# Optimization experiments

Measured on AMD Instinct MI355X. Metric: run time of the kernel, lower is better.

The kernel has to match this reference:

```python
import jax, jax.numpy as jnp
import numpy as np

H, KVH, HD, HID = 16, 8, 128, 2048
GROUPS = H // KVH
THETA = 10000.0
EPS = 1e-6


def _rms_norm(x, w):
    # x: (..., HD), norm in fp32 like Qwen3RMSNorm
    xf = x.astype(jnp.float32)
    var = jnp.mean(xf * xf, axis=-1, keepdims=True)
    return (xf * jax.lax.rsqrt(var + EPS)).astype(x.dtype) * w


def _rope_cos_sin(position_ids, dtype):
    # position_ids: (B, S) int
    inv_freq = 1.0 / (THETA ** (jnp.arange(0, HD, 2, dtype=jnp.float32) / HD))  # (HD/2,)
    freqs = position_ids.astype(jnp.float32)[..., None] * inv_freq  # (B, S, HD/2)
    emb = jnp.concatenate([freqs, freqs], axis=-1)  # (B, S, HD)
    return jnp.cos(emb).astype(dtype), jnp.sin(emb).astype(dtype)


def _rotate_half(x):
    x1, x2 = jnp.split(x, 2, axis=-1)
    return jnp.concatenate([-x2, x1], axis=-1)


def _apply_rope(q, k, cos, sin):
    # q,k: (B, h, S, HD); cos,sin: (B, S, HD) -> broadcast over head dim
    cos = cos[:, None, :, :]
    sin = sin[:, None, :, :]
    q = q * cos + _rotate_half(q) * sin
    k = k * cos + _rotate_half(k) * sin
    return q, k


def setup_inputs() -> dict:
    key = jax.random.key(0)
    ks = jax.random.split(key, 10)
    B, S, L = 1, 2048, 2048
    w = 0.02
    return {
        "hidden_states": jax.random.normal(ks[0], (B, S, HID), jnp.float32),
        "context": jax.random.normal(ks[1], (B, L, HID), jnp.float32),
        "position_ids": jnp.arange(S, dtype=jnp.int64)[None, :].repeat(B, axis=0),
        "Wq": jax.random.normal(ks[2], (H * HD, HID), jnp.float32) * w,
        "Wk": jax.random.normal(ks[3], (KVH * HD, HID), jnp.float32) * w,
        "Wv": jax.random.normal(ks[4], (KVH * HD, HID), jnp.float32) * w,
        "Wo": jax.random.normal(ks[5], (HID, H * HD), jnp.float32) * w,
        "Wk_ctx": jax.random.normal(ks[6], (KVH * HD, HID), jnp.float32) * w,
        "Wv_ctx": jax.random.normal(ks[7], (KVH * HD, HID), jnp.float32) * w,
        "q_norm_w": jnp.ones((HD,), jnp.float32),
        "k_norm_w": jnp.ones((HD,), jnp.float32),
    }


def reference(hidden_states, context, position_ids, Wq, Wk, Wv, Wo, Wk_ctx, Wv_ctx, q_norm_w, k_norm_w):
    B, S, _ = hidden_states.shape
    L = context.shape[1]
    scaling = HD ** -0.5

    Q = (hidden_states @ Wq.T).reshape(B, S, H, HD).transpose(0, 2, 1, 3)    # (B,H,S,HD)
    K = (hidden_states @ Wk.T).reshape(B, S, KVH, HD).transpose(0, 2, 1, 3)  # (B,KVH,S,HD)
    V = (hidden_states @ Wv.T).reshape(B, S, KVH, HD).transpose(0, 2, 1, 3)

    Q = _rms_norm(Q, q_norm_w)
    K = _rms_norm(K, k_norm_w)

    cos, sin = _rope_cos_sin(position_ids, Q.dtype)
    Q, K = _apply_rope(Q, K, cos, sin)

    K_ctx = (context @ Wk_ctx.T).reshape(B, L, KVH, HD).transpose(0, 2, 1, 3)
    V_ctx = (context @ Wv_ctx.T).reshape(B, L, KVH, HD).transpose(0, 2, 1, 3)

    K_full = jnp.concatenate([K_ctx, K], axis=2)  # (B,KVH,L+S,HD)
    V_full = jnp.concatenate([V_ctx, V], axis=2)
    K_full = jnp.repeat(K_full, GROUPS, axis=1)   # (B,H,L+S,HD)
    V_full = jnp.repeat(V_full, GROUPS, axis=1)

    attn = jnp.einsum("bhsd,bhtd->bhst", Q, K_full) * scaling  # (B,H,S,L+S)
    attn = jax.nn.softmax(attn.astype(jnp.float32), axis=-1).astype(Q.dtype)
    out = jnp.einsum("bhst,bhtd->bhsd", attn, V_full)          # (B,H,S,HD)
    out = out.transpose(0, 2, 1, 3).reshape(B, S, H * HD)
    return out @ Wo.T
```

## Files before the change

### kernel.cpp

```cpp
#include <hip/hip_runtime.h>

typedef __bf16 bf16_t;
typedef __attribute__((ext_vector_type(8))) __bf16 bf16x8;
typedef __attribute__((ext_vector_type(4))) __bf16 bf16x4;
typedef __attribute__((ext_vector_type(4))) float f32x4;

#define LDA_PAD 72

__device__ __forceinline__ bf16x8 ld8(const float* g) {
  f32x4 a = *(const f32x4*)g;
  f32x4 b = *(const f32x4*)(g + 4);
  bf16x8 r;
  r[0] = (bf16_t)a[0]; r[1] = (bf16_t)a[1]; r[2] = (bf16_t)a[2]; r[3] = (bf16_t)a[3];
  r[4] = (bf16_t)b[0]; r[5] = (bf16_t)b[1]; r[6] = (bf16_t)b[2]; r[7] = (bf16_t)b[3];
  return r;
}
__device__ __forceinline__ bf16x8 ld8(const bf16_t* g) { return *(const bf16x8*)g; }

__global__ __launch_bounds__(256) void cvt_wo(const float* __restrict__ src,
                                              bf16_t* __restrict__ dst) {
  const size_t off = (size_t)(blockIdx.x * 256 + threadIdx.x) * 8;
  *(bf16x8*)(dst + off) = ld8(src + off);
}

template<typename TI>
__global__ __launch_bounds__(256) void proj_all(
    const TI* __restrict__ hs, const TI* __restrict__ ctx,
    const TI* __restrict__ Wq, const TI* __restrict__ Wk,
    const TI* __restrict__ Wv, const TI* __restrict__ Wkc,
    const TI* __restrict__ Wvc,
    bf16_t* __restrict__ Qb, bf16_t* __restrict__ Kb, bf16_t* __restrict__ Vt)
{
  __shared__ __align__(16) bf16_t lA[128 * LDA_PAD];
  __shared__ __align__(16) bf16_t lB[128 * LDA_PAD];
  const int tid = threadIdx.x, wave = tid >> 6, lane = tid & 63;
  const int quad = lane >> 4, lc = lane & 15;
  const int u = blockIdx.x;
  const int xcd = u & 7, v = u >> 3;
  const int op = v >> 5, w = v & 31;
  const int nh = w >> 4, mt0 = w & 15;
  const int n0 = (xcd + nh * 8) * 128, m0 = mt0 * 128;
  const TI* A; const TI* B;
  if (op == 0) { A = hs; B = Wq + (size_t)n0 * 2048; }
  else {
    A = (op == 1) ? ctx : hs;
    const TI* WK = (op == 1) ? Wkc : Wk;
    const TI* WV = (op == 1) ? Wvc : Wv;
    B = (n0 < 1024) ? WK + (size_t)n0 * 2048 : WV + (size_t)(n0 - 1024) * 2048;
  }
  const int mw = (wave >> 1) * 64, nw = (wave & 1) * 64;
  const int lr8 = lane >> 3, lc8 = (lane & 7) * 8;

  f32x4 acc[4][4];
#pragma unroll
  for (int i = 0; i < 4; ++i)
#pragma unroll
    for (int j = 0; j < 4; ++j) acc[i][j] = (f32x4){0.f, 0.f, 0.f, 0.f};

  bf16x8 pa[4], pb[4];
#pragma unroll
  for (int i = 0; i < 4; ++i) {
    const int row = (wave + 4 * i) * 8 + lr8;
    pa[i] = ld8(A + (size_t)(m0 + row) * 2048 + lc8);
    pb[i] = ld8(B + (size_t)row * 2048 + lc8);
  }

  for (int k0 = 0; k0 < 2048; k0 += 64) {
    __syncthreads();
#pragma unroll
    for (int i = 0; i < 4; ++i) {
      const int row = (wave + 4 * i) * 8 + lr8;
      *(bf16x8*)(lA + row * LDA_PAD + lc8) = pa[i];
      *(bf16x8*)(lB + row * LDA_PAD + lc8) = pb[i];
    }
    __syncthreads();
    if (k0 + 64 < 2048) {
      const int kn = k0 + 64;
#pragma unroll
      for (int i = 0; i < 4; ++i) {
        const int row = (wave + 4 * i) * 8 + lr8;
        pa[i] = ld8(A + (size_t)(m0 + row) * 2048 + kn + lc8);
        pb[i] = ld8(B + (size_t)row * 2048 + kn + lc8);
      }
    }
#pragma unroll
    for (int kk = 0; kk < 2; ++kk) {
      bf16x8 af[4], bfv[4];
#pragma unroll
      for (int mt = 0; mt < 4; ++mt)
        af[mt] = *(const bf16x8*)(lA + (mw + mt * 16 + lc) * LDA_PAD + kk * 32 + quad * 8);
#pragma unroll
      for (int nt = 0; nt < 4; ++nt)
        bfv[nt] = *(const bf16x8*)(lB + (nw + nt * 16 + lc) * LDA_PAD + kk * 32 + quad * 8);
#pragma unroll
      for (int mt = 0; mt < 4; ++mt)
#pragma unroll
        for (int nt = 0; nt < 4; ++nt)
          acc[mt][nt] = __builtin_amdgcn_mfma_f32_16x16x32_bf16(af[mt], bfv[nt], acc[mt][nt], 0, 0, 0);
    }
  }

  if (op == 0) {
#pragma unroll
    for (int mt = 0; mt < 4; ++mt)
#pragma unroll
      for (int nt = 0; nt < 4; ++nt)
#pragma unroll
        for (int r = 0; r < 4; ++r)
          Qb[(size_t)(m0 + mw + mt * 16 + quad * 4 + r) * 2048 + n0 + nw + nt * 16 + lc]
              = (bf16_t)acc[mt][nt][r];
  } else {
    const int t_off = (op == 1) ? 0 : 2048;
    if (n0 < 1024) {
#pragma unroll
      for (int mt = 0; mt < 4; ++mt)
#pragma unroll
        for (int nt = 0; nt < 4; ++nt)
#pragma unroll
          for (int r = 0; r < 4; ++r) {
            const int n = n0 + nw + nt * 16 + lc;
            const int kvh = n >> 7, dd = n & 127;
            const int t = t_off + m0 + mw + mt * 16 + quad * 4 + r;
            Kb[((size_t)kvh * 4096 + t) * 128 + dd] = (bf16_t)acc[mt][nt][r];
          }
    } else {
#pragma unroll
      for (int mt = 0; mt < 4; ++mt)
#pragma unroll
        for (int nt = 0; nt < 4; ++nt) {
          const int n = n0 - 1024 + nw + nt * 16 + lc;
          const int kvh = n >> 7, dd = n & 127;
          const int t = t_off + m0 + mw + mt * 16 + quad * 4;
          bf16x4 pk;
#pragma unroll
          for (int r = 0; r < 4; ++r) pk[r] = (bf16_t)acc[mt][nt][r];
          *(bf16x4*)(Vt + ((size_t)kvh * 128 + dd) * 4096 + t) = pk;
        }
    }
  }
}

__global__ __launch_bounds__(256) void normrope(
    bf16_t* __restrict__ Q, bf16_t* __restrict__ Kb,
    const float* __restrict__ qw, const float* __restrict__ kw)
{
  const int wave = threadIdx.x >> 6, lane = threadIdx.x & 63;
  const int row = blockIdx.x * 4 + wave;
  bf16_t* p; const float* w; int pos;
  if (row < 32768) {
    const int s = row >> 4, hh = row & 15;
    p = Q + (size_t)s * 2048 + hh * 128; w = qw; pos = s;
  } else {
    const int rk = row - 32768;
    const int s = rk >> 3, hh = rk & 7;
    p = Kb + ((size_t)hh * 4096 + 2048 + s) * 128; w = kw; pos = s;
  }
  const float x1 = (float)p[lane], x2 = (float)p[lane + 64];
  float ss = x1 * x1 + x2 * x2;
#pragma unroll
  for (int m = 1; m < 64; m <<= 1) ss += __shfl_xor(ss, m, 64);
  const float inv = rsqrtf(ss * (1.0f / 128.0f) + 1e-6f);
  const float y1 = x1 * inv * w[lane];
  const float y2 = x2 * inv * w[lane + 64];
  const float freq = (float)pos * exp2f((float)lane * (-13.287712379549449f / 64.0f));
  const float cb = cosf(freq), sb = sinf(freq);
  p[lane]      = (bf16_t)(y1 * cb - y2 * sb);
  p[lane + 64] = (bf16_t)(y2 * cb + y1 * sb);
}

template<int SPLIT>
__global__ __launch_bounds__(512, 4) void attn_kernel(
    const bf16_t* __restrict__ Q, const bf16_t* __restrict__ Kb,
    const bf16_t* __restrict__ Vt, bf16_t* __restrict__ O,
    float* __restrict__ Of, float* __restrict__ Lf)
{
  __shared__ __align__(16) char lK[64 * 256];
  __shared__ __align__(16) char lV[128 * 128];
  __shared__ __align__(16) char lP[8 * 2048];
  const int tid = threadIdx.x, wave = tid >> 6, lane = tid & 63;
  const int quad = lane >> 4, lc = lane & 15;
  const int bid = blockIdx.x;
  const int hk = bid & 7, qt = (bid >> 3) & 15, hsel = (bid >> 7) & 1;
  const int half = SPLIT ? (bid >> 8) : 0;
  const int h = hk * 2 + hsel;
  const int mrow0 = qt * 128 + wave * 16;
  const int tbase = half * 2048;
  const int tend = tbase + (SPLIT ? 2048 : 4096);
  const float cexp = 0.08838834764831845f * 1.4426950408889634f;

  bf16x8 qf[4];
  {
    const bf16_t* qb = Q + (size_t)(mrow0 + lc) * 2048 + h * 128 + quad * 8;
#pragma unroll
    for (int ks = 0; ks < 4; ++ks) qf[ks] = *(const bf16x8*)(qb + ks * 32);
  }
  float rs[4] = {0.f, 0.f, 0.f, 0.f};
  f32x4 oacc[8];
#pragma unroll
  for (int ot = 0; ot < 8; ++ot) oacc[ot] = (f32x4){0.f, 0.f, 0.f, 0.f};

  bf16x8 kp[2], vp[2];
  auto load_tile = [&](int t0) {
    const bf16_t* Kt = Kb + ((size_t)hk * 4096 + t0) * 128;
    const bf16_t* Vb = Vt + (size_t)hk * 524288 + t0;
#pragma unroll
    for (int i = 0; i < 2; ++i) {
      const int idx = wave * 2 + i;
      kp[i] = *(const bf16x8*)(Kt + (size_t)(idx * 4 + quad) * 128 + lc * 8);
      vp[i] = *(const bf16x8*)(Vb + (size_t)(idx * 8 + (lane >> 3)) * 4096 + (lane & 7) * 8);
    }
  };
  load_tile(tbase);

  char* lPw = lP + wave * 2048;
  const int sw_rd = (lc & 7) << 4;

  for (int t0 = tbase; t0 < tend; t0 += 64) {
    __syncthreads();
#pragma unroll
    for (int i = 0; i < 2; ++i) {
      const int idx = wave * 2 + i;
      const int kr = idx * 4 + quad;
      *(bf16x8*)(lK + kr * 256 + ((lc * 16) ^ ((kr & 7) << 4))) = kp[i];
      const int vr = idx * 8 + (lane >> 3);
      *(bf16x8*)(lV + vr * 128 + (((lane & 7) * 16) ^ ((vr & 7) << 4))) = vp[i];
    }
    __syncthreads();
    if (t0 + 64 < tend) load_tile(t0 + 64);

    f32x4 s[4];
#pragma unroll
    for (int nt = 0; nt < 4; ++nt) {
      f32x4 a = (f32x4){0.f, 0.f, 0.f, 0.f};
#pragma unroll
      for (int ks = 0; ks < 4; ++ks) {
        bf16x8 kf = *(const bf16x8*)(lK + (nt * 16 + lc) * 256 + ((ks * 64 + quad * 16) ^ sw_rd));
        a = __builtin_amdgcn_mfma_f32_16x16x32_bf16(qf[ks], kf, a, 0, 0, 0);
      }
      s[nt] = a;
    }

#pragma unroll
    for (int nt = 0; nt < 4; ++nt)
#pragma unroll
      for (int r = 0; r < 4; ++r) {
        const float pv = exp2f(s[nt][r] * cexp);
        rs[r] += pv;
        const int pr = quad * 4 + r;
        *(bf16_t*)(lPw + pr * 128 + ((nt * 32 + lc * 2) ^ ((pr & 7) << 4))) = (bf16_t)pv;
      }

#pragma unroll
    for (int ks2 = 0; ks2 < 2; ++ks2) {
      bf16x8 pf = *(const bf16x8*)(lPw + lc * 128 + ((ks2 * 64 + quad * 16) ^ sw_rd));
#pragma unroll
      for (int ot = 0; ot < 8; ++ot) {
        bf16x8 vf = *(const bf16x8*)(lV + (ot * 16 + lc) * 128 + ((ks2 * 64 + quad * 16) ^ sw_rd));
        oacc[ot] = __builtin_amdgcn_mfma_f32_16x16x32_bf16(pf, vf, oacc[ot], 0, 0, 0);
      }
    }
  }

  float l_r[4];
#pragma unroll
  for (int r = 0; r < 4; ++r) {
    float vv = rs[r];
    vv += __shfl_xor(vv, 1, 64);
    vv += __shfl_xor(vv, 2, 64);
    vv += __shfl_xor(vv, 4, 64);
    vv += __shfl_xor(vv, 8, 64);
    l_r[r] = vv;
  }
  if (SPLIT) {
    float* Oh = Of + (size_t)half * 4194304;
#pragma unroll
    for (int ot = 0; ot < 8; ++ot)
#pragma unroll
      for (int r = 0; r < 4; ++r)
        Oh[(size_t)(mrow0 + quad * 4 + r) * 2048 + h * 128 + ot * 16 + lc] = oacc[ot][r];
    if (lc == 0) {
      float* Lh = Lf + half * 32768 + h * 2048 + mrow0;
#pragma unroll
      for (int r = 0; r < 4; ++r) Lh[quad * 4 + r] = l_r[r];
    }
  } else {
#pragma unroll
    for (int ot = 0; ot < 8; ++ot)
#pragma unroll
      for (int r = 0; r < 4; ++r)
        O[(size_t)(mrow0 + quad * 4 + r) * 2048 + h * 128 + ot * 16 + lc]
            = (bf16_t)(oacc[ot][r] / l_r[r]);
  }
}

__global__ __launch_bounds__(256) void combine(
    const float* __restrict__ Of, const float* __restrict__ Lf,
    bf16_t* __restrict__ Ob)
{
  const int b = blockIdx.x;
  const int hk = b & 7, idx = b >> 3;
  const int h = hk * 2 + (idx & 1), sg = idx >> 1;
  const int t = threadIdx.x;
  const int s = sg * 16 + (t >> 4), d = (t & 15) * 8;
  const size_t e = (size_t)s * 2048 + h * 128 + d;
  const float l = Lf[h * 2048 + s] + Lf[32768 + h * 2048 + s];
  const float inv = 1.0f / l;
  f32x4 a0 = *(const f32x4*)(Of + e);
  f32x4 a1 = *(const f32x4*)(Of + e + 4);
  f32x4 b0 = *(const f32x4*)(Of + 4194304 + e);
  f32x4 b1 = *(const f32x4*)(Of + 4194304 + e + 4);
  bf16x8 rr;
#pragma unroll
  for (int j = 0; j < 4; ++j) {
    rr[j]     = (bf16_t)((a0[j] + b0[j]) * inv);
    rr[4 + j] = (bf16_t)((a1[j] + b1[j]) * inv);
  }
  *(bf16x8*)(Ob + e) = rr;
}

template<typename TB>
__global__ __launch_bounds__(256) void gemm_o(
    const bf16_t* __restrict__ A, const TB* __restrict__ Bw,
    float* __restrict__ C)
{
  __shared__ __align__(16) bf16_t lA[128 * LDA_PAD];
  __shared__ __align__(16) bf16_t lB[64 * LDA_PAD];
  const int tid = threadIdx.x, wave = tid >> 6, lane = tid & 63;
  const int quad = lane >> 4, lc = lane & 15;
  const int bid = blockIdx.x;
  const int xcd = bid & 7, v = bid >> 3;
  const int nh = v >> 4, mt0 = v & 15;
  const int n0 = (xcd + nh * 8) * 64, m0 = mt0 * 128;
  const int mw = (wave >> 1) * 64, nw = (wave & 1) * 32;
  const int lr8 = lane >> 3, lc8 = (lane & 7) * 8;

  f32x4 acc[4][2];
#pragma unroll
  for (int i = 0; i < 4; ++i)
#pragma unroll
    for (int j = 0; j < 2; ++j) acc[i][j] = (f32x4){0.f, 0.f, 0.f, 0.f};

  bf16x8 pa[4], pb[2];
#pragma unroll
  for (int i = 0; i < 4; ++i)
    pa[i] = ld8(A + (size_t)(m0 + (wave + 4 * i) * 8 + lr8) * 2048 + lc8);
#pragma unroll
  for (int i = 0; i < 2; ++i)
    pb[i] = ld8(Bw + (size_t)(n0 + i * 32 + wave * 8 + lr8) * 2048 + lc8);

  for (int k0 = 0; k0 < 2048; k0 += 64) {
    __syncthreads();
#pragma unroll
    for (int i = 0; i < 4; ++i)
      *(bf16x8*)(lA + ((wave + 4 * i) * 8 + lr8) * LDA_PAD + lc8) = pa[i];
#pragma unroll
    for (int i = 0; i < 2; ++i)
      *(bf16x8*)(lB + (i * 32 + wave * 8 + lr8) * LDA_PAD + lc8) = pb[i];
    __syncthreads();
    if (k0 + 64 < 2048) {
      const int kn = k0 + 64;
#pragma unroll
      for (int i = 0; i < 4; ++i)
        pa[i] = ld8(A + (size_t)(m0 + (wave + 4 * i) * 8 + lr8) * 2048 + kn + lc8);
#pragma unroll
      for (int i = 0; i < 2; ++i)
        pb[i] = ld8(Bw + (size_t)(n0 + i * 32 + wave * 8 + lr8) * 2048 + kn + lc8);
    }
#pragma unroll
    for (int kk = 0; kk < 2; ++kk) {
      bf16x8 af[4], bfv[2];
#pragma unroll
      for (int mt = 0; mt < 4; ++mt)
        af[mt] = *(const bf16x8*)(lA + (mw + mt * 16 + lc) * LDA_PAD + kk * 32 + quad * 8);
#pragma unroll
      for (int nt = 0; nt < 2; ++nt)
        bfv[nt] = *(const bf16x8*)(lB + (nw + nt * 16 + lc) * LDA_PAD + kk * 32 + quad * 8);
#pragma unroll
      for (int mt = 0; mt < 4; ++mt)
#pragma unroll
        for (int nt = 0; nt < 2; ++nt)
          acc[mt][nt] = __builtin_amdgcn_mfma_f32_16x16x32_bf16(af[mt], bfv[nt], acc[mt][nt], 0, 0, 0);
    }
  }
#pragma unroll
  for (int mt = 0; mt < 4; ++mt)
#pragma unroll
    for (int nt = 0; nt < 2; ++nt)
#pragma unroll
      for (int r = 0; r < 4; ++r)
        C[(size_t)(m0 + mw + mt * 16 + quad * 4 + r) * 2048 + n0 + nw + nt * 16 + lc]
            = acc[mt][nt][r];
}

extern "C" void kernel_launch(void* const* d_in, const int* in_sizes, int n_in,
                              void* d_out, int out_size, void* d_ws, size_t ws_size,
                              hipStream_t stream)
{
  const float* hs  = (const float*)d_in[0];
  const float* ctx = (const float*)d_in[1];
  const float* Wq  = (const float*)d_in[3];
  const float* Wk  = (const float*)d_in[4];
  const float* Wv  = (const float*)d_in[5];
  const float* Wo  = (const float*)d_in[6];
  const float* Wkc = (const float*)d_in[7];
  const float* Wvc = (const float*)d_in[8];
  const float* qw  = (const float*)d_in[9];
  const float* kw  = (const float*)d_in[10];

  bf16_t* Kb = (bf16_t*)d_out;
  bf16_t* Vt = Kb + (size_t)4 * 1024 * 1024;
  bf16_t* wsb = (bf16_t*)d_ws;
  const bool fast = ws_size >= (size_t)64 * 1024 * 1024;

  dim3 blk(256), ablk(512);
  if (fast) {
    float*  Of    = (float*)wsb;
    float*  Lfp   = (float*)(wsb + (size_t)16 * 1024 * 1024);
    bf16_t* Wo_b  = wsb + (size_t)40 * 524288;
    bf16_t* Qb    = wsb + (size_t)48 * 524288;
    bf16_t* Ob    = wsb + (size_t)56 * 524288;
    cvt_wo<<<dim3(2048), blk, 0, stream>>>(Wo, Wo_b);
    proj_all<float><<<dim3(768), blk, 0, stream>>>(
        hs, ctx, Wq, Wk, Wv, Wkc, Wvc, Qb, Kb, Vt);
    normrope<<<dim3(12288), blk, 0, stream>>>(Qb, Kb, qw, kw);
    attn_kernel<1><<<dim3(512), ablk, 0, stream>>>(Qb, Kb, Vt, nullptr, Of, Lfp);
    combine<<<dim3(2048), blk, 0, stream>>>(Of, Lfp, Ob);
    gemm_o<bf16_t><<<dim3(512), blk, 0, stream>>>(Ob, Wo_b, (float*)d_out);
  } else {
    bf16_t* Qb = wsb;
    bf16_t* Ob = wsb + (size_t)8 * 524288;
    proj_all<float><<<dim3(768), blk, 0, stream>>>(
        hs, ctx, Wq, Wk, Wv, Wkc, Wvc, Qb, Kb, Vt);
    normrope<<<dim3(12288), blk, 0, stream>>>(Qb, Kb, qw, kw);
    attn_kernel<0><<<dim3(256), ablk, 0, stream>>>(Qb, Kb, Vt, Ob, nullptr, nullptr);
    gemm_o<float><<<dim3(512), blk, 0, stream>>>(Ob, Wo, (float*)d_out);
  }
}
```

Measured before the change: 411.8 us.

## Fuse split-KV combine into output GEMM and pre-convert activations instead of Wo

Removes the separate combine kernel by merging the two split-KV partial outputs and normalizing by the summed softmax denominators inside the A-tile staging of the output projection GEMM. Wo is now read directly as fp32 instead of being converted to bf16 first. Hidden states and context are pre-converted to bf16 so the projection GEMM reads half-width activations. This trades two launches and an intermediate bf16 buffer for heavier fp32 loads of Of and Wo inside the GEMM main loop, repeated across N tiles.

```diff
diff --git a/kernel.cpp b/kernel.cpp
--- a/kernel.cpp
+++ b/kernel.cpp
@@ -17,18 +17,25 @@
 }
 __device__ __forceinline__ bf16x8 ld8(const bf16_t* g) { return *(const bf16x8*)g; }
 
-__global__ __launch_bounds__(256) void cvt_wo(const float* __restrict__ src,
-                                              bf16_t* __restrict__ dst) {
-  const size_t off = (size_t)(blockIdx.x * 256 + threadIdx.x) * 8;
-  *(bf16x8*)(dst + off) = ld8(src + off);
-}
-
-template<typename TI>
+__global__ __launch_bounds__(256) void cvt2(
+    const float* __restrict__ hs, const float* __restrict__ ctx,
+    bf16_t* __restrict__ hs_b, bf16_t* __restrict__ ctx_b) {
+  const int g = blockIdx.x * 256 + threadIdx.x;
+  if (g < 524288) {
+    const size_t off = (size_t)g * 8;
+    *(bf16x8*)(hs_b + off) = ld8(hs + off);
+  } else {
+    const size_t off = (size_t)(g - 524288) * 8;
+    *(bf16x8*)(ctx_b + off) = ld8(ctx + off);
+  }
+}
+
+template<typename TA>
 __global__ __launch_bounds__(256) void proj_all(
-    const TI* __restrict__ hs, const TI* __restrict__ ctx,
-    const TI* __restrict__ Wq, const TI* __restrict__ Wk,
-    const TI* __restrict__ Wv, const TI* __restrict__ Wkc,
-    const TI* __restrict__ Wvc,
+    const TA* __restrict__ hs, const TA* __restrict__ ctx,
+    const float* __restrict__ Wq, const float* __restrict__ Wk,
+    const float* __restrict__ Wv, const float* __restrict__ Wkc,
+    const float* __restrict__ Wvc,
     bf16_t* __restrict__ Qb, bf16_t* __restrict__ Kb, bf16_t* __restrict__ Vt)
 {
   __shared__ __align__(16) bf16_t lA[128 * LDA_PAD];
@@ -40,12 +47,12 @@
   const int op = v >> 5, w = v & 31;
   const int nh = w >> 4, mt0 = w & 15;
   const int n0 = (xcd + nh * 8) * 128, m0 = mt0 * 128;
-  const TI* A; const TI* B;
+  const TA* A; const float* B;
   if (op == 0) { A = hs; B = Wq + (size_t)n0 * 2048; }
   else {
     A = (op == 1) ? ctx : hs;
-    const TI* WK = (op == 1) ? Wkc : Wk;
-    const TI* WV = (op == 1) ? Wvc : Wv;
+    const float* WK = (op == 1) ? Wkc : Wk;
+    const float* WV = (op == 1) ? Wvc : Wv;
     B = (n0 < 1024) ? WK + (size_t)n0 * 2048 : WV + (size_t)(n0 - 1024) * 2048;
   }
   const int mw = (wave >> 1) * 64, nw = (wave & 1) * 64;
@@ -293,34 +300,101 @@
   }
 }
 
-__global__ __launch_bounds__(256) void combine(
+__global__ __launch_bounds__(256) void gemm_of(
     const float* __restrict__ Of, const float* __restrict__ Lf,
-    bf16_t* __restrict__ Ob)
+    const float* __restrict__ Wo, float* __restrict__ C)
 {
-  const int b = blockIdx.x;
-  const int hk = b & 7, idx = b >> 3;
-  const int h = hk * 2 + (idx & 1), sg = idx >> 1;
-  const int t = threadIdx.x;
-  const int s = sg * 16 + (t >> 4), d = (t & 15) * 8;
-  const size_t e = (size_t)s * 2048 + h * 128 + d;
-  const float l = Lf[h * 2048 + s] + Lf[32768 + h * 2048 + s];
-  const float inv = 1.0f / l;
-  f32x4 a0 = *(const f32x4*)(Of + e);
-  f32x4 a1 = *(const f32x4*)(Of + e + 4);
-  f32x4 b0 = *(const f32x4*)(Of + 4194304 + e);
-  f32x4 b1 = *(const f32x4*)(Of + 4194304 + e + 4);
-  bf16x8 rr;
-#pragma unroll
-  for (int j = 0; j < 4; ++j) {
-    rr[j]     = (bf16_t)((a0[j] + b0[j]) * inv);
-    rr[4 + j] = (bf16_t)((a1[j] + b1[j]) * inv);
-  }
-  *(bf16x8*)(Ob + e) = rr;
-}
-
-template<typename TB>
+  __shared__ __align__(16) bf16_t lA[128 * LDA_PAD];
+  __shared__ __align__(16) bf16_t lB[64 * LDA_PAD];
+  const int tid = threadIdx.x, wave = tid >> 6, lane = tid & 63;
+  const int quad = lane >> 4, lc = lane & 15;
+  const int bid = blockIdx.x;
+  const int xcd = bid & 7, v = bid >> 3;
+  const int nh = v >> 4, mt0 = v & 15;
+  const int n0 = (xcd + nh * 8) * 64, m0 = mt0 * 128;
+  const int mw = (wave >> 1) * 64, nw = (wave & 1) * 32;
+  const int lr8 = lane >> 3, lc8 = (lane & 7) * 8;
+
+  int rowA[4];
+#pragma unroll
+  for (int i = 0; i < 4; ++i) rowA[i] = m0 + (wave + 4 * i) * 8 + lr8;
+
+  auto stage_a = [&](int i, int kc) -> bf16x8 {
+    const size_t e = (size_t)rowA[i] * 2048 + kc + lc8;
+    f32x4 a0 = *(const f32x4*)(Of + e);
+    f32x4 a1 = *(const f32x4*)(Of + e + 4);
+    f32x4 b0 = *(const f32x4*)(Of + 4194304 + e);
+    f32x4 b1 = *(const f32x4*)(Of + 4194304 + e + 4);
+    const int hb = (kc >> 7) * 2048 + rowA[i];
+    const float l = Lf[hb] + Lf[32768 + hb];
+    const float inv = 1.0f / l;
+    bf16x8 r;
+#pragma unroll
+    for (int j = 0; j < 4; ++j) {
+      r[j]     = (bf16_t)((a0[j] + b0[j]) * inv);
+      r[4 + j] = (bf16_t)((a1[j] + b1[j]) * inv);
+    }
+    return r;
+  };
+
+  f32x4 acc[4][2];
+#pragma unroll
+  for (int i = 0; i < 4; ++i)
+#pragma unroll
+    for (int j = 0; j < 2; ++j) acc[i][j] = (f32x4){0.f, 0.f, 0.f, 0.f};
+
+  bf16x8 pa[4], pb[2];
+#pragma unroll
+  for (int i = 0; i < 4; ++i) pa[i] = stage_a(i, 0);
+#pragma unroll
+  for (int i = 0; i < 2; ++i)
+    pb[i] = ld8(Wo + (size_t)(n0 + i * 32 + wave * 8 + lr8) * 2048 + lc8);
+
+  for (int k0 = 0; k0 < 2048; k0 += 64) {
+    __syncthreads();
+#pragma unroll
+    for (int i = 0; i < 4; ++i)
+      *(bf16x8*)(lA + ((wave + 4 * i) * 8 + lr8) * LDA_PAD + lc8) = pa[i];
+#pragma unroll
+    for (int i = 0; i < 2; ++i)
+      *(bf16x8*)(lB + (i * 32 + wave * 8 + lr8) * LDA_PAD + lc8) = pb[i];
+    __syncthreads();
+    if (k0 + 64 < 2048) {
+      const int kn = k0 + 64;
+#pragma unroll
+      for (int i = 0; i < 4; ++i) pa[i] = stage_a(i, kn);
+#pragma unroll
+      for (int i = 0; i < 2; ++i)
+        pb[i] = ld8(Wo + (size_t)(n0 + i * 32 + wave * 8 + lr8) * 2048 + kn + lc8);
+    }
+#pragma unroll
+    for (int kk = 0; kk < 2; ++kk) {
+      bf16x8 af[4], bfv[2];
+#pragma unroll
+      for (int mt = 0; mt < 4; ++mt)
+        af[mt] = *(const bf16x8*)(lA + (mw + mt * 16 + lc) * LDA_PAD + kk * 32 + quad * 8);
+#pragma unroll
+      for (int nt = 0; nt < 2; ++nt)
+        bfv[nt] = *(const bf16x8*)(lB + (nw + nt * 16 + lc) * LDA_PAD + kk * 32 + quad * 8);
+#pragma unroll
+      for (int mt = 0; mt < 4; ++mt)
+#pragma unroll
+        for (int nt = 0; nt < 2; ++nt)
+          acc[mt][nt] = __builtin_amdgcn_mfma_f32_16x16x32_bf16(af[mt], bfv[nt], acc[mt][nt], 0, 0, 0);
+    }
+  }
+#pragma unroll
+  for (int mt = 0; mt < 4; ++mt)
+#pragma unroll
+    for (int nt = 0; nt < 2; ++nt)
+#pragma unroll
+      for (int r = 0; r < 4; ++r)
+        C[(size_t)(m0 + mw + mt * 16 + quad * 4 + r) * 2048 + n0 + nw + nt * 16 + lc]
+            = acc[mt][nt][r];
+}
+
 __global__ __launch_bounds__(256) void gemm_o(
-    const bf16_t* __restrict__ A, const TB* __restrict__ Bw,
+    const bf16_t* __restrict__ A, const float* __restrict__ Bw,
     float* __restrict__ C)
 {
   __shared__ __align__(16) bf16_t lA[128 * LDA_PAD];
@@ -414,18 +488,17 @@
 
   dim3 blk(256), ablk(512);
   if (fast) {
-    float*  Of    = (float*)wsb;
-    float*  Lfp   = (float*)(wsb + (size_t)16 * 1024 * 1024);
-    bf16_t* Wo_b  = wsb + (size_t)40 * 524288;
-    bf16_t* Qb    = wsb + (size_t)48 * 524288;
-    bf16_t* Ob    = wsb + (size_t)56 * 524288;
-    cvt_wo<<<dim3(2048), blk, 0, stream>>>(Wo, Wo_b);
-    proj_all<float><<<dim3(768), blk, 0, stream>>>(
-        hs, ctx, Wq, Wk, Wv, Wkc, Wvc, Qb, Kb, Vt);
+    bf16_t* hs_b  = wsb;
+    bf16_t* ctx_b = wsb + (size_t)8  * 524288;
+    bf16_t* Qb    = wsb + (size_t)16 * 524288;
+    float*  Of    = (float*)(wsb + (size_t)24 * 524288);
+    float*  Lfp   = (float*)(wsb + (size_t)56 * 524288);
+    cvt2<<<dim3(4096), blk, 0, stream>>>(hs, ctx, hs_b, ctx_b);
+    proj_all<bf16_t><<<dim3(768), blk, 0, stream>>>(
+        hs_b, ctx_b, Wq, Wk, Wv, Wkc, Wvc, Qb, Kb, Vt);
     normrope<<<dim3(12288), blk, 0, stream>>>(Qb, Kb, qw, kw);
     attn_kernel<1><<<dim3(512), ablk, 0, stream>>>(Qb, Kb, Vt, nullptr, Of, Lfp);
-    combine<<<dim3(2048), blk, 0, stream>>>(Of, Lfp, Ob);
-    gemm_o<bf16_t><<<dim3(512), blk, 0, stream>>>(Ob, Wo_b, (float*)d_out);
+    gemm_of<<<dim3(512), blk, 0, stream>>>(Of, Lfp, Wo, (float*)d_out);
   } else {
     bf16_t* Qb = wsb;
     bf16_t* Ob = wsb + (size_t)8 * 524288;
@@ -433,6 +506,6 @@
         hs, ctx, Wq, Wk, Wv, Wkc, Wvc, Qb, Kb, Vt);
     normrope<<<dim3(12288), blk, 0, stream>>>(Qb, Kb, qw, kw);
     attn_kernel<0><<<dim3(256), ablk, 0, stream>>>(Qb, Kb, Vt, Ob, nullptr, nullptr);
-    gemm_o<float><<<dim3(512), blk, 0, stream>>>(Ob, Wo, (float*)d_out);
-  }
-}
+    gemm_o<<<dim3(512), blk, 0, stream>>>(Ob, Wo, (float*)d_out);
+  }
+}
```

Measured after the change: 442.2 us. +7.4%, slower.
